# Performance work log

Measured on AMD Instinct MI355X. Metric: run time of the kernel, lower is better.

Reference implementation:

```python
import jax, jax.numpy as jnp
import numpy as np

HIDDEN = 1024
HEADS = 16
HEAD_DIM = HIDDEN // HEADS


def setup_inputs() -> dict:
    key = jax.random.key(0)
    kx, kw = jax.random.split(key)
    x = jax.random.normal(kx, (1, 4096, HIDDEN), dtype=jnp.float32)
    # torch Linear weight is [out, in]; we store as [in, out] for x @ W
    W_qkv = jax.random.normal(kw, (HIDDEN, 3 * HIDDEN), dtype=jnp.float32) * (HIDDEN ** -0.5)
    return {"x": x, "W_qkv": W_qkv}


def reference(x, W_qkv):
    B, T, _ = x.shape
    qkv = x @ W_qkv                                    # [B, T, 3*HIDDEN]
    qkv = qkv.reshape(B, T, 3, HEADS, HEAD_DIM)
    qkv = jnp.transpose(qkv, (2, 0, 3, 1, 4))          # [3, B, H, T, Dh]
    q, k, v = qkv[0], qkv[1], qkv[2]
    scale = HEAD_DIM ** -0.5
    attn = jnp.einsum("bhqd,bhkd->bhqk", q, k) * scale  # [B, H, T, T] materialized (naive)
    attn = jax.nn.softmax(attn, axis=-1)
    out = jnp.einsum("bhqk,bhkd->bhqd", attn, v)        # [B, H, T, Dh]
    out = jnp.transpose(out, (0, 2, 1, 3)).reshape(B, T, HIDDEN)
    return out
```

## Files before the change

### kernel.cpp

```cpp
#include <hip/hip_runtime.h>

#define SEQ 4096
#define HID 1024
#define NH  16
#define DH  64
#define N3  3072

typedef __attribute__((ext_vector_type(4))) float floatx4;
typedef __attribute__((ext_vector_type(8))) short shortx8;
typedef __attribute__((ext_vector_type(4))) short shortx4;

__device__ __forceinline__ short f2bf(float f) {
    return (short)((__builtin_bit_cast(unsigned, f) + 0x8000u) >> 16);
}
__device__ __forceinline__ unsigned pk2bf(float a, float b) {
    unsigned ua = __builtin_bit_cast(unsigned, a) + 0x8000u;
    unsigned ub = __builtin_bit_cast(unsigned, b) + 0x8000u;
    return (ua >> 16) | (ub & 0xFFFF0000u);
}
__device__ __forceinline__ shortx4 pk4bf(float a, float b, float c, float d) {
    union { unsigned u[2]; shortx4 s; } x;
    x.u[0] = pk2bf(a, b);
    x.u[1] = pk2bf(c, d);
    return x.s;
}

#if __has_builtin(__builtin_amdgcn_exp2f)
#define fexp2 __builtin_amdgcn_exp2f
#else
#define fexp2 exp2f
#endif

#define mfma32 __builtin_amdgcn_mfma_f32_16x16x32_bf16

#if __has_builtin(__builtin_amdgcn_mfma_f32_16x16x16bf16_1k)
__device__ __forceinline__ floatx4 mfma16(shortx4 a, shortx4 b, floatx4 c) {
    return __builtin_amdgcn_mfma_f32_16x16x16bf16_1k(a, b, c, 0, 0, 0);
}
#else
__device__ __forceinline__ floatx4 mfma16(shortx4 a, shortx4 b, floatx4 c) {
    asm volatile("v_mfma_f32_16x16x16_bf16 %0, %1, %2, %0\n\ts_nop 7\n\ts_nop 4"
                 : "+v"(c) : "v"(a), "v"(b));
    return c;
}
#endif

__device__ __forceinline__ void gll16(const short* g, short* l) {
    __builtin_amdgcn_global_load_lds(
        (const __attribute__((address_space(1))) unsigned*)g,
        (__attribute__((address_space(3))) unsigned*)l, 16, 0, 0);
}

__global__ __launch_bounds__(256) void convert_x(
    const float* __restrict__ x, short* __restrict__ Xb)
{
    size_t i = (size_t)blockIdx.x * 256 + threadIdx.x;
    float4 v = *(const float4*)&x[i * 4];
    shortx4 b = pk4bf(v.x, v.y, v.z, v.w);
    *(shortx4*)&Xb[i * 4] = b;
}

__global__ __launch_bounds__(256) void transpose_W(
    const float* __restrict__ W, short* __restrict__ Wt)
{
    __shared__ short Ws[128 * 40];
    const int t  = threadIdx.x;
    const int n0 = blockIdx.x * 128;
    const int k0 = blockIdx.y * 32;
    #pragma unroll
    for (int i = 0; i < 4; i++) {
        int idx = t + i * 256;
        int k = idx >> 5, c4 = idx & 31;
        float4 v = *(const float4*)&W[(size_t)(k0 + k) * N3 + n0 + c4 * 4];
        Ws[(c4 * 4 + 0) * 40 + k] = f2bf(v.x);
        Ws[(c4 * 4 + 1) * 40 + k] = f2bf(v.y);
        Ws[(c4 * 4 + 2) * 40 + k] = f2bf(v.z);
        Ws[(c4 * 4 + 3) * 40 + k] = f2bf(v.w);
    }
    __syncthreads();
    #pragma unroll
    for (int i = 0; i < 2; i++) {
        int idx = t + i * 256;
        int n = idx >> 2, seg = idx & 3;
        shortx8 g = *(const shortx8*)&Ws[n * 40 + seg * 8];
        *(shortx8*)&Wt[(size_t)(n0 + n) * HID + k0 + seg * 8] = g;
    }
}

#define LDC 136
__global__ __launch_bounds__(256) void qkv_gemm(
    const short* __restrict__ Xb, const short* __restrict__ Wt,
    short* __restrict__ Qb, short* __restrict__ Kb, short* __restrict__ Vb)
{
    __shared__ short SM[18432];
    short* As = SM;
    short* Bs = SM + 128 * 64;
    const int tid  = threadIdx.x;
    const int n0   = blockIdx.x * 128;
    const int m0   = blockIdx.y * 128;
    const int lane = tid & 63;
    const int wid  = tid >> 6;
    const int wm   = (wid >> 1) * 64;
    const int wn   = (wid & 1) * 64;
    const int l15  = lane & 15;
    const int quad = lane >> 4;

    floatx4 acc[4][4];
    #pragma unroll
    for (int i = 0; i < 4; i++)
        #pragma unroll
        for (int j = 0; j < 4; j++)
            acc[i][j] = (floatx4){0.f, 0.f, 0.f, 0.f};

    const int arow = tid >> 3, ac = tid & 7;
    const int swk  = (ac ^ (arow & 7)) << 3;
    const short* ag = Xb + (size_t)(m0 + arow) * HID + swk;
    const short* bg = Wt + (size_t)(n0 + arow) * HID + swk;
    short* al = As + (size_t)(tid & 192) * 8;
    short* bl = Bs + (size_t)(tid & 192) * 8;
    const int r7 = l15 & 7;

    for (int k0 = 0; k0 < HID; k0 += 64) {
        #pragma unroll
        for (int i = 0; i < 4; i++)
            gll16(ag + (size_t)i * 32 * HID + k0, al + i * 2048);
        #pragma unroll
        for (int i = 0; i < 4; i++)
            gll16(bg + (size_t)i * 32 * HID + k0, bl + i * 2048);
        __syncthreads();
        #pragma unroll
        for (int kh = 0; kh < 2; kh++) {
            shortx8 af[4], bf[4];
            #pragma unroll
            for (int t = 0; t < 4; t++) {
                int R = wm + t * 16 + l15;
                af[t] = *(const shortx8*)&As[(R << 6) + ((((kh << 2) + quad) ^ r7) << 3)];
                int Rb = wn + t * 16 + l15;
                bf[t] = *(const shortx8*)&Bs[(Rb << 6) + ((((kh << 2) + quad) ^ r7) << 3)];
            }
            #pragma unroll
            for (int tm = 0; tm < 4; tm++)
                #pragma unroll
                for (int tn = 0; tn < 4; tn++)
                    acc[tm][tn] = mfma32(af[tm], bf[tn], acc[tm][tn], 0, 0, 0);
        }
        __syncthreads();
    }

    short* Cs = SM;
    const float sc = (n0 < 1024) ? 0.18033688011112042f : 1.0f;
    #pragma unroll
    for (int tm = 0; tm < 4; tm++)
        #pragma unroll
        for (int tn = 0; tn < 4; tn++)
            #pragma unroll
            for (int r = 0; r < 4; r++)
                Cs[(wm + tm * 16 + quad * 4 + r) * LDC + wn + tn * 16 + l15] =
                    f2bf(acc[tm][tn][r] * sc);
    __syncthreads();
    short* base = (n0 < 1024) ? Qb : (n0 < 2048 ? Kb : Vb);
    const int h0 = (n0 & 1023) >> 6;
    #pragma unroll
    for (int j = 0; j < 8; j++) {
        int idx = tid + j * 256;
        int row = idx >> 4, col = (idx & 15) * 8;
        shortx8 v = *(const shortx8*)&Cs[row * LDC + col];
        *(shortx8*)&base[((size_t)(h0 + (col >> 6)) * SEQ + m0 + row) * DH + (col & 63)] = v;
    }
}

__global__ __launch_bounds__(256) void transpose_V(
    const short* __restrict__ Vb, short* __restrict__ Vt)
{
    __shared__ short Ts[64 * 72];
    const int t  = threadIdx.x;
    const int t0 = blockIdx.x * 64;
    const int h  = blockIdx.y;
    #pragma unroll
    for (int i = 0; i < 2; i++) {
        int idx = t + i * 256;
        int r = idx >> 3, seg = idx & 7;
        shortx8 g = *(const shortx8*)&Vb[((size_t)h * SEQ + t0 + r) * DH + seg * 8];
        *(shortx8*)&Ts[r * 72 + seg * 8] = g;
    }
    __syncthreads();
    #pragma unroll
    for (int i = 0; i < 2; i++) {
        int idx = t + i * 256;
        int d = idx >> 3, p8 = idx & 7;
        shortx8 g;
        #pragma unroll
        for (int j = 0; j < 8; j++) {
            int p  = p8 * 8 + j;
            int u  = ((p >> 2) & 3) * 16 + ((p >> 4) & 3) * 4 + (p & 3);
            g[j] = Ts[u * 72 + d];
        }
        *(shortx8*)&Vt[((size_t)h * DH + d) * SEQ + t0 + p8 * 8] = g;
    }
}

__global__ __launch_bounds__(256) void flash_attn(
    const short* __restrict__ Qb, const short* __restrict__ Kb,
    const short* __restrict__ Vt, float* __restrict__ out,
    float* __restrict__ Opart, float* __restrict__ Lpart,
    int kpc, int nit, int final)
{
    __shared__ short Ks[2][64 * 64];
    __shared__ short Vs[2][64 * 64];
    const int tid  = threadIdx.x;
    const int lane = tid & 63;
    const int l15  = lane & 15;
    const int quad = lane >> 4;
    const int h    = blockIdx.y;
    const int ch   = blockIdx.z;
    const int q0   = blockIdx.x * 128 + (tid >> 6) * 32;
    const int tstart = ch * kpc;
    const int sw   = (l15 & 7) << 3;
    const shortx4 kOnes = {(short)0x3F80, (short)0x3F80, (short)0x3F80, (short)0x3F80};

    const short* qp = Qb + ((size_t)h * SEQ + q0 + l15) * DH;
    shortx8 qf00 = *(const shortx8*)(qp + quad * 8);
    shortx8 qf01 = *(const shortx8*)(qp + 32 + quad * 8);
    shortx8 qf10 = *(const shortx8*)(qp + 16 * DH + quad * 8);
    shortx8 qf11 = *(const shortx8*)(qp + 16 * DH + 32 + quad * 8);

    floatx4 oacc[2][4];
    #pragma unroll
    for (int s = 0; s < 2; s++)
        #pragma unroll
        for (int dn = 0; dn < 4; dn++)
            oacc[s][dn] = (floatx4){0.f, 0.f, 0.f, 0.f};
    floatx4 lacc0 = {0.f, 0.f, 0.f, 0.f}, lacc1 = {0.f, 0.f, 0.f, 0.f};

    const int i0 = tid, i1 = tid + 256;
    const int r0 = i0 >> 3, c0 = i0 & 7;
    const int r1 = i1 >> 3, c1 = i1 & 7;
    const short* kt0 = Kb + ((size_t)h * SEQ + r0) * DH + c0 * 8;
    const short* kt1 = Kb + ((size_t)h * SEQ + r1) * DH + c1 * 8;
    const short* vt0 = Vt + ((size_t)h * DH + r0) * SEQ + c0 * 8;
    const short* vt1 = Vt + ((size_t)h * DH + r1) * SEQ + c1 * 8;
    const int lo0 = (r0 << 6) + ((c0 ^ (r0 & 7)) << 3);
    const int lo1 = (r1 << 6) + ((c1 ^ (r1 & 7)) << 3);

    shortx8 kr0, kr1, vr0, vr1;
    kr0 = *(const shortx8*)(kt0 + (size_t)tstart * DH);
    kr1 = *(const shortx8*)(kt1 + (size_t)tstart * DH);
    vr0 = *(const shortx8*)(vt0 + tstart);
    vr1 = *(const shortx8*)(vt1 + tstart);
    *(shortx8*)&Ks[0][lo0] = kr0;  *(shortx8*)&Ks[0][lo1] = kr1;
    *(shortx8*)&Vs[0][lo0] = vr0;  *(shortx8*)&Vs[0][lo1] = vr1;

    for (int it = 0; it < nit; it++) {
        __syncthreads();
        if (it + 1 < nit) {
            int tn0 = tstart + (it + 1) * 64;
            kr0 = *(const shortx8*)(kt0 + (size_t)tn0 * DH);
            kr1 = *(const shortx8*)(kt1 + (size_t)tn0 * DH);
            vr0 = *(const shortx8*)(vt0 + tn0);
            vr1 = *(const shortx8*)(vt1 + tn0);
        }
        const short* ks = Ks[it & 1];
        const short* vs = Vs[it & 1];

        floatx4 st0[4], st1[4];
        #pragma unroll
        for (int tn = 0; tn < 4; tn++) {
            int k0a = (((tn * 16 + l15) << 6) + sw) ^ (quad << 3);
            shortx8 kf0 = *(const shortx8*)&ks[k0a];
            shortx8 kf1 = *(const shortx8*)&ks[k0a ^ 32];
            floatx4 a0 = {0.f, 0.f, 0.f, 0.f};
            a0 = mfma32(kf0, qf00, a0, 0, 0, 0);
            a0 = mfma32(kf1, qf01, a0, 0, 0, 0);
            st0[tn] = a0;
            floatx4 a1 = {0.f, 0.f, 0.f, 0.f};
            a1 = mfma32(kf0, qf10, a1, 0, 0, 0);
            a1 = mfma32(kf1, qf11, a1, 0, 0, 0);
            st1[tn] = a1;
        }

        shortx4 pb0[4], pb1[4];
        #pragma unroll
        for (int tn = 0; tn < 4; tn++) {
            float e0 = fexp2(st0[tn][0]), e1 = fexp2(st0[tn][1]);
            float e2 = fexp2(st0[tn][2]), e3 = fexp2(st0[tn][3]);
            pb0[tn] = pk4bf(e0, e1, e2, e3);
            float f0 = fexp2(st1[tn][0]), f1 = fexp2(st1[tn][1]);
            float f2 = fexp2(st1[tn][2]), f3 = fexp2(st1[tn][3]);
            pb1[tn] = pk4bf(f0, f1, f2, f3);
        }

        #pragma unroll
        for (int tn = 0; tn < 4; tn++) {
            lacc0 = mfma16(pb0[tn], kOnes, lacc0);
            lacc1 = mfma16(pb1[tn], kOnes, lacc1);
        }

        #pragma unroll
        for (int dn = 0; dn < 4; dn++) {
            int row = dn * 16 + l15;
            int bse = row << 6;
            int rr  = row & 7;
            shortx8 va = *(const shortx8*)&vs[bse + ((((quad << 1)    ) ^ rr) << 3)];
            shortx8 vb = *(const shortx8*)&vs[bse + ((((quad << 1) | 1) ^ rr) << 3)];
            shortx4 v0 = {va[0], va[1], va[2], va[3]};
            shortx4 v1 = {va[4], va[5], va[6], va[7]};
            shortx4 v2 = {vb[0], vb[1], vb[2], vb[3]};
            shortx4 v3 = {vb[4], vb[5], vb[6], vb[7]};
            oacc[0][dn] = mfma16(pb0[0], v0, oacc[0][dn]);
            oacc[0][dn] = mfma16(pb0[1], v1, oacc[0][dn]);
            oacc[0][dn] = mfma16(pb0[2], v2, oacc[0][dn]);
            oacc[0][dn] = mfma16(pb0[3], v3, oacc[0][dn]);
            oacc[1][dn] = mfma16(pb1[0], v0, oacc[1][dn]);
            oacc[1][dn] = mfma16(pb1[1], v1, oacc[1][dn]);
            oacc[1][dn] = mfma16(pb1[2], v2, oacc[1][dn]);
            oacc[1][dn] = mfma16(pb1[3], v3, oacc[1][dn]);
        }

        if (it + 1 < nit) {
            int b = (it + 1) & 1;
            *(shortx8*)&Ks[b][lo0] = kr0;  *(shortx8*)&Ks[b][lo1] = kr1;
            *(shortx8*)&Vs[b][lo0] = vr0;  *(shortx8*)&Vs[b][lo1] = vr1;
        }
    }

    if (final) {
        #pragma unroll
        for (int r = 0; r < 4; r++) {
            float rl0 = 1.0f / lacc0[r], rl1 = 1.0f / lacc1[r];
            int query = q0 + quad * 4 + r;
            float* d0 = out + (size_t)query * HID + h * DH + l15;
            float* d1 = d0 + (size_t)16 * HID;
            #pragma unroll
            for (int dn = 0; dn < 4; dn++) {
                d0[dn * 16] = oacc[0][dn][r] * rl0;
                d1[dn * 16] = oacc[1][dn][r] * rl1;
            }
        }
    } else {
        #pragma unroll
        for (int r = 0; r < 4; r++) {
            int query = q0 + quad * 4 + r;
            float* d0 = Opart + ((size_t)ch * SEQ + query) * HID + h * DH + l15;
            float* d1 = d0 + (size_t)16 * HID;
            #pragma unroll
            for (int dn = 0; dn < 4; dn++) {
                d0[dn * 16] = oacc[0][dn][r];
                d1[dn * 16] = oacc[1][dn][r];
            }
        }
        if (l15 == 0) {
            float* lp = Lpart + ((size_t)ch * NH + h) * SEQ + q0;
            #pragma unroll
            for (int r = 0; r < 4; r++) {
                lp[quad * 4 + r]      = lacc0[r];
                lp[16 + quad * 4 + r] = lacc1[r];
            }
        }
    }
}

__global__ __launch_bounds__(256) void combine(
    const float* __restrict__ Opart, const float* __restrict__ Lpart,
    float* __restrict__ out, int chn)
{
    size_t i = ((size_t)blockIdx.x * 256 + threadIdx.x) * 4;
    int q = (int)(i >> 10);
    int h = ((int)i & 1023) >> 6;
    float4 o = {0.f, 0.f, 0.f, 0.f};
    float l = 0.f;
    for (int c = 0; c < chn; c++) {
        float4 p = *(const float4*)&Opart[(size_t)c * SEQ * HID + i];
        o.x += p.x; o.y += p.y; o.z += p.z; o.w += p.w;
        l += Lpart[((size_t)c * NH + h) * SEQ + q];
    }
    float rl = 1.0f / l;
    float4 r = {o.x * rl, o.y * rl, o.z * rl, o.w * rl};
    *(float4*)&out[i] = r;
}

extern "C" void kernel_launch(void* const* d_in, const int* in_sizes, int n_in,
                              void* d_out, int out_size, void* d_ws, size_t ws_size,
                              hipStream_t stream) {
    const float* x = (const float*)d_in[0];
    const float* W = (const float*)d_in[1];
    float* out = (float*)d_out;

    short* Xb = (short*)d_ws;
    short* Wt = Xb + (size_t)SEQ * HID;
    short* Qb = Wt + (size_t)N3 * HID;
    short* Kb = Qb + (size_t)NH * SEQ * DH;
    short* Vb = Kb + (size_t)NH * SEQ * DH;
    short* Vt = Xb;
    float* Opart = (float*)(Vb + (size_t)NH * SEQ * DH);

    const size_t need = 39845888ull
                      + 2ull * SEQ * HID * 4
                      + 2ull * NH * SEQ * 4;
    const int chn = (ws_size >= need) ? 2 : 1;
    float* Lpart = Opart + (size_t)chn * SEQ * HID;
    const int kpc = SEQ / chn, nit = kpc / 64;

    convert_x  <<<dim3(SEQ * HID / 1024), 256, 0, stream>>>(x, Xb);
    transpose_W<<<dim3(N3 / 128, HID / 32), 256, 0, stream>>>(W, Wt);
    qkv_gemm   <<<dim3(N3 / 128, SEQ / 128), 256, 0, stream>>>(Xb, Wt, Qb, Kb, Vb);
    transpose_V<<<dim3(SEQ / 64, NH), 256, 0, stream>>>(Vb, Vt);
    flash_attn <<<dim3(SEQ / 128, NH, chn), 256, 0, stream>>>(
        Qb, Kb, Vt, out, Opart, Lpart, kpc, nit, chn == 1);
    if (chn > 1)
        combine<<<dim3(SEQ * HID / 1024), 256, 0, stream>>>(Opart, Lpart, out, chn);
}
```

Measured before the change: 229.7 us.

## Use 16x16x32 MFMA for PV, async LDS loads, swap GEMM grid, split keys 4-way

The attention kernel now runs the P·V and row-sum products with the wider 16x16x32 bf16 MFMA instead of 16x16x16, and permutes K rows and V columns to match the new P fragment layout. K/V tiles are fetched with global_load_lds straight into shared memory instead of staging through registers. The QKV GEMM grid is transposed so consecutive blocks walk along M, and the key dimension is split into 4 chunks instead of 2 when the workspace allows. This trades fewer MFMA issues and register staging for more partial-output traffic in the combine step, and relies on the reordered key layout being correct.

```diff
diff --git a/kernel.cpp b/kernel.cpp
--- a/kernel.cpp
+++ b/kernel.cpp
@@ -32,18 +32,6 @@
 #endif
 
 #define mfma32 __builtin_amdgcn_mfma_f32_16x16x32_bf16
-
-#if __has_builtin(__builtin_amdgcn_mfma_f32_16x16x16bf16_1k)
-__device__ __forceinline__ floatx4 mfma16(shortx4 a, shortx4 b, floatx4 c) {
-    return __builtin_amdgcn_mfma_f32_16x16x16bf16_1k(a, b, c, 0, 0, 0);
-}
-#else
-__device__ __forceinline__ floatx4 mfma16(shortx4 a, shortx4 b, floatx4 c) {
-    asm volatile("v_mfma_f32_16x16x16_bf16 %0, %1, %2, %0\n\ts_nop 7\n\ts_nop 4"
-                 : "+v"(c) : "v"(a), "v"(b));
-    return c;
-}
-#endif
 
 __device__ __forceinline__ void gll16(const short* g, short* l) {
     __builtin_amdgcn_global_load_lds(
@@ -96,8 +84,8 @@
     short* As = SM;
     short* Bs = SM + 128 * 64;
     const int tid  = threadIdx.x;
-    const int n0   = blockIdx.x * 128;
-    const int m0   = blockIdx.y * 128;
+    const int m0   = blockIdx.x * 128;
+    const int n0   = blockIdx.y * 128;
     const int lane = tid & 63;
     const int wid  = tid >> 6;
     const int wm   = (wid >> 1) * 64;
@@ -187,15 +175,11 @@
     #pragma unroll
     for (int i = 0; i < 2; i++) {
         int idx = t + i * 256;
-        int d = idx >> 3, p8 = idx & 7;
+        int d = idx >> 3, tseg = idx & 7;
         shortx8 g;
         #pragma unroll
-        for (int j = 0; j < 8; j++) {
-            int p  = p8 * 8 + j;
-            int u  = ((p >> 2) & 3) * 16 + ((p >> 4) & 3) * 4 + (p & 3);
-            g[j] = Ts[u * 72 + d];
-        }
-        *(shortx8*)&Vt[((size_t)h * DH + d) * SEQ + t0 + p8 * 8] = g;
+        for (int j = 0; j < 8; j++) g[j] = Ts[(tseg * 8 + j) * 72 + d];
+        *(shortx8*)&Vt[((size_t)h * DH + d) * SEQ + t0 + tseg * 8] = g;
     }
 }
 
@@ -205,8 +189,8 @@
     float* __restrict__ Opart, float* __restrict__ Lpart,
     int kpc, int nit, int final)
 {
-    __shared__ short Ks[2][64 * 64];
-    __shared__ short Vs[2][64 * 64];
+    __shared__ short Ks[2][4096];
+    __shared__ short Vs[2][4096];
     const int tid  = threadIdx.x;
     const int lane = tid & 63;
     const int l15  = lane & 15;
@@ -215,8 +199,8 @@
     const int ch   = blockIdx.z;
     const int q0   = blockIdx.x * 128 + (tid >> 6) * 32;
     const int tstart = ch * kpc;
-    const int sw   = (l15 & 7) << 3;
-    const shortx4 kOnes = {(short)0x3F80, (short)0x3F80, (short)0x3F80, (short)0x3F80};
+    const shortx8 ones8 = {(short)0x3F80, (short)0x3F80, (short)0x3F80, (short)0x3F80,
+                           (short)0x3F80, (short)0x3F80, (short)0x3F80, (short)0x3F80};
 
     const short* qp = Qb + ((size_t)h * SEQ + q0 + l15) * DH;
     shortx8 qf00 = *(const shortx8*)(qp + quad * 8);
@@ -232,32 +216,28 @@
             oacc[s][dn] = (floatx4){0.f, 0.f, 0.f, 0.f};
     floatx4 lacc0 = {0.f, 0.f, 0.f, 0.f}, lacc1 = {0.f, 0.f, 0.f, 0.f};
 
-    const int i0 = tid, i1 = tid + 256;
-    const int r0 = i0 >> 3, c0 = i0 & 7;
-    const int r1 = i1 >> 3, c1 = i1 & 7;
-    const short* kt0 = Kb + ((size_t)h * SEQ + r0) * DH + c0 * 8;
-    const short* kt1 = Kb + ((size_t)h * SEQ + r1) * DH + c1 * 8;
-    const short* vt0 = Vt + ((size_t)h * DH + r0) * SEQ + c0 * 8;
-    const short* vt1 = Vt + ((size_t)h * DH + r1) * SEQ + c1 * 8;
-    const int lo0 = (r0 << 6) + ((c0 ^ (r0 & 7)) << 3);
-    const int lo1 = (r1 << 6) + ((c1 ^ (r1 & 7)) << 3);
-
-    shortx8 kr0, kr1, vr0, vr1;
-    kr0 = *(const shortx8*)(kt0 + (size_t)tstart * DH);
-    kr1 = *(const shortx8*)(kt1 + (size_t)tstart * DH);
-    vr0 = *(const shortx8*)(vt0 + tstart);
-    vr1 = *(const shortx8*)(vt1 + tstart);
-    *(shortx8*)&Ks[0][lo0] = kr0;  *(shortx8*)&Ks[0][lo1] = kr1;
-    *(shortx8*)&Vs[0][lo0] = vr0;  *(shortx8*)&Vs[0][lo1] = vr1;
+    const int rK   = tid >> 3, sK = tid & 7;
+    const int key0 = 8 * ((rK >> 2) & 3) + 4 * ((rK >> 4) & 1) + (rK & 3);
+    const int swo  = (sK ^ (rK & 7)) << 3;
+    const short* kg = Kb + ((size_t)h * SEQ + tstart + key0) * DH + swo;
+    const short* vg = Vt + ((size_t)h * DH + rK) * SEQ + tstart + swo;
+    const int wslot = (tid & 192) * 8;
+
+    gll16(kg,            &Ks[0][wslot]);
+    gll16(kg + 32 * DH,  &Ks[0][wslot + 2048]);
+    gll16(vg,            &Vs[0][wslot]);
+    gll16(vg + 32 * SEQ, &Vs[0][wslot + 2048]);
+    kg += 64 * DH;  vg += 64;
 
     for (int it = 0; it < nit; it++) {
         __syncthreads();
         if (it + 1 < nit) {
-            int tn0 = tstart + (it + 1) * 64;
-            kr0 = *(const shortx8*)(kt0 + (size_t)tn0 * DH);
-            kr1 = *(const shortx8*)(kt1 + (size_t)tn0 * DH);
-            vr0 = *(const shortx8*)(vt0 + tn0);
-            vr1 = *(const shortx8*)(vt1 + tn0);
+            int b = (it + 1) & 1;
+            gll16(kg,            &Ks[b][wslot]);
+            gll16(kg + 32 * DH,  &Ks[b][wslot + 2048]);
+            gll16(vg,            &Vs[b][wslot]);
+            gll16(vg + 32 * SEQ, &Vs[b][wslot + 2048]);
+            kg += 64 * DH;  vg += 64;
         }
         const short* ks = Ks[it & 1];
         const short* vs = Vs[it & 1];
@@ -265,9 +245,10 @@
         floatx4 st0[4], st1[4];
         #pragma unroll
         for (int tn = 0; tn < 4; tn++) {
-            int k0a = (((tn * 16 + l15) << 6) + sw) ^ (quad << 3);
-            shortx8 kf0 = *(const shortx8*)&ks[k0a];
-            shortx8 kf1 = *(const shortx8*)&ks[k0a ^ 32];
+            int R = tn * 16 + l15;
+            int off = (R << 6) + ((quad ^ (R & 7)) << 3);
+            shortx8 kf0 = *(const shortx8*)&ks[off];
+            shortx8 kf1 = *(const shortx8*)&ks[off ^ 32];
             floatx4 a0 = {0.f, 0.f, 0.f, 0.f};
             a0 = mfma32(kf0, qf00, a0, 0, 0, 0);
             a0 = mfma32(kf1, qf01, a0, 0, 0, 0);
@@ -278,48 +259,37 @@
             st1[tn] = a1;
         }
 
-        shortx4 pb0[4], pb1[4];
-        #pragma unroll
-        for (int tn = 0; tn < 4; tn++) {
-            float e0 = fexp2(st0[tn][0]), e1 = fexp2(st0[tn][1]);
-            float e2 = fexp2(st0[tn][2]), e3 = fexp2(st0[tn][3]);
-            pb0[tn] = pk4bf(e0, e1, e2, e3);
-            float f0 = fexp2(st1[tn][0]), f1 = fexp2(st1[tn][1]);
-            float f2 = fexp2(st1[tn][2]), f3 = fexp2(st1[tn][3]);
-            pb1[tn] = pk4bf(f0, f1, f2, f3);
-        }
-
-        #pragma unroll
-        for (int tn = 0; tn < 4; tn++) {
-            lacc0 = mfma16(pb0[tn], kOnes, lacc0);
-            lacc1 = mfma16(pb1[tn], kOnes, lacc1);
-        }
+        union { unsigned u[4]; shortx8 s; } pa00, pa01, pa10, pa11;
+        #pragma unroll
+        for (int half = 0; half < 2; half++) {
+            int ta = half * 2, tb = half * 2 + 1;
+            unsigned* d0 = half ? pa01.u : pa00.u;
+            unsigned* d1 = half ? pa11.u : pa10.u;
+            d0[0] = pk2bf(fexp2(st0[ta][0]), fexp2(st0[ta][1]));
+            d0[1] = pk2bf(fexp2(st0[ta][2]), fexp2(st0[ta][3]));
+            d0[2] = pk2bf(fexp2(st0[tb][0]), fexp2(st0[tb][1]));
+            d0[3] = pk2bf(fexp2(st0[tb][2]), fexp2(st0[tb][3]));
+            d1[0] = pk2bf(fexp2(st1[ta][0]), fexp2(st1[ta][1]));
+            d1[1] = pk2bf(fexp2(st1[ta][2]), fexp2(st1[ta][3]));
+            d1[2] = pk2bf(fexp2(st1[tb][0]), fexp2(st1[tb][1]));
+            d1[3] = pk2bf(fexp2(st1[tb][2]), fexp2(st1[tb][3]));
+        }
+
+        lacc0 = mfma32(pa00.s, ones8, lacc0, 0, 0, 0);
+        lacc0 = mfma32(pa01.s, ones8, lacc0, 0, 0, 0);
+        lacc1 = mfma32(pa10.s, ones8, lacc1, 0, 0, 0);
+        lacc1 = mfma32(pa11.s, ones8, lacc1, 0, 0, 0);
 
         #pragma unroll
         for (int dn = 0; dn < 4; dn++) {
             int row = dn * 16 + l15;
-            int bse = row << 6;
-            int rr  = row & 7;
-            shortx8 va = *(const shortx8*)&vs[bse + ((((quad << 1)    ) ^ rr) << 3)];
-            shortx8 vb = *(const shortx8*)&vs[bse + ((((quad << 1) | 1) ^ rr) << 3)];
-            shortx4 v0 = {va[0], va[1], va[2], va[3]};
-            shortx4 v1 = {va[4], va[5], va[6], va[7]};
-            shortx4 v2 = {vb[0], vb[1], vb[2], vb[3]};
-            shortx4 v3 = {vb[4], vb[5], vb[6], vb[7]};
-            oacc[0][dn] = mfma16(pb0[0], v0, oacc[0][dn]);
-            oacc[0][dn] = mfma16(pb0[1], v1, oacc[0][dn]);
-            oacc[0][dn] = mfma16(pb0[2], v2, oacc[0][dn]);
-            oacc[0][dn] = mfma16(pb0[3], v3, oacc[0][dn]);
-            oacc[1][dn] = mfma16(pb1[0], v0, oacc[1][dn]);
-            oacc[1][dn] = mfma16(pb1[1], v1, oacc[1][dn]);
-            oacc[1][dn] = mfma16(pb1[2], v2, oacc[1][dn]);
-            oacc[1][dn] = mfma16(pb1[3], v3, oacc[1][dn]);
-        }
-
-        if (it + 1 < nit) {
-            int b = (it + 1) & 1;
-            *(shortx8*)&Ks[b][lo0] = kr0;  *(shortx8*)&Ks[b][lo1] = kr1;
-            *(shortx8*)&Vs[b][lo0] = vr0;  *(shortx8*)&Vs[b][lo1] = vr1;
+            int off = (row << 6) + ((quad ^ (row & 7)) << 3);
+            shortx8 va = *(const shortx8*)&vs[off];
+            shortx8 vb = *(const shortx8*)&vs[off ^ 32];
+            oacc[0][dn] = mfma32(pa00.s, va, oacc[0][dn], 0, 0, 0);
+            oacc[0][dn] = mfma32(pa01.s, vb, oacc[0][dn], 0, 0, 0);
+            oacc[1][dn] = mfma32(pa10.s, va, oacc[1][dn], 0, 0, 0);
+            oacc[1][dn] = mfma32(pa11.s, vb, oacc[1][dn], 0, 0, 0);
         }
     }
 
@@ -394,15 +364,15 @@
     float* Opart = (float*)(Vb + (size_t)NH * SEQ * DH);
 
     const size_t need = 39845888ull
-                      + 2ull * SEQ * HID * 4
-                      + 2ull * NH * SEQ * 4;
-    const int chn = (ws_size >= need) ? 2 : 1;
+                      + 4ull * SEQ * HID * 4
+                      + 4ull * NH * SEQ * 4;
+    const int chn = (ws_size >= need) ? 4 : 1;
     float* Lpart = Opart + (size_t)chn * SEQ * HID;
     const int kpc = SEQ / chn, nit = kpc / 64;
 
     convert_x  <<<dim3(SEQ * HID / 1024), 256, 0, stream>>>(x, Xb);
     transpose_W<<<dim3(N3 / 128, HID / 32), 256, 0, stream>>>(W, Wt);
-    qkv_gemm   <<<dim3(N3 / 128, SEQ / 128), 256, 0, stream>>>(Xb, Wt, Qb, Kb, Vb);
+    qkv_gemm   <<<dim3(SEQ / 128, N3 / 128), 256, 0, stream>>>(Xb, Wt, Qb, Kb, Vb);
     transpose_V<<<dim3(SEQ / 64, NH), 256, 0, stream>>>(Vb, Vt);
     flash_attn <<<dim3(SEQ / 128, NH, chn), 256, 0, stream>>>(
         Qb, Kb, Vt, out, Opart, Lpart, kpc, nit, chn == 1);
```

After: 214.5 us. 1.07x faster.
